# Kernel tuning notes

Hardware: AMD Instinct MI355X
Metric: run time of the kernel (lower is better)

The kernel has to match this reference:

```python
import jax, jax.numpy as jnp
import numpy as np

D_MODEL = 1024
N_HEADS = 16
D_HEAD = 64
TOTAL = N_HEADS * D_HEAD


def setup_inputs() -> dict:
    key = jax.random.key(0)
    k1, k2, k3 = jax.random.split(key, 3)
    x = jax.random.normal(k1, (2, 2048, D_MODEL), dtype=jnp.float32)
    W_qkv = jax.random.normal(k2, (3 * TOTAL, D_MODEL), dtype=jnp.float32) * 0.02
    W_out = jax.random.normal(k3, (D_MODEL, TOTAL), dtype=jnp.float32) * 0.02
    return {"x": x, "W_qkv": W_qkv, "W_out": W_out}


def reference(x, W_qkv, W_out):
    B, T, D = x.shape
    scale = D_HEAD ** -0.5
    qkv = jnp.einsum('btd,ed->bte', x, W_qkv)  # [B,T,3*TOTAL]
    q, k, v = jnp.split(qkv, 3, axis=-1)
    def heads(t):
        return t.reshape(B, T, N_HEADS, D_HEAD).transpose(0, 2, 1, 3)  # [B,H,T,Dh]
    q, k, v = heads(q), heads(k), heads(v)
    scores = jnp.einsum('bhqd,bhkd->bhqk', q, k) * scale
    causal = jnp.tril(jnp.ones((T, T), dtype=bool))
    scores = jnp.where(causal[None, None], scores, -jnp.inf)
    attn = jax.nn.softmax(scores, axis=-1)
    out = jnp.einsum('bhqk,bhkd->bhqd', attn, v)
    out = out.transpose(0, 2, 1, 3).reshape(B, T, TOTAL)
    return jnp.einsum('bte,de->btd', out, W_out)
```

## Files before the change

### kernel.cpp

```cpp
#include <hip/hip_runtime.h>
#include <hip/hip_bf16.h>

typedef __attribute__((ext_vector_type(4))) float f32x4;
typedef __attribute__((ext_vector_type(8))) short s16x8;
typedef __attribute__((ext_vector_type(4))) short s16x4;

#define DEV static __device__ __forceinline__

DEV unsigned short f2bf(float f) {
    unsigned int u = __builtin_bit_cast(unsigned int, f);
    u += 0x7fffu + ((u >> 16) & 1u);
    return (unsigned short)(u >> 16);
}

#if __has_builtin(__builtin_amdgcn_exp2f)
#define EXP2(x) __builtin_amdgcn_exp2f(x)
#else
#define EXP2(x) exp2f(x)
#endif

DEV unsigned int pack2(float a, float b) {
#if __has_builtin(__builtin_amdgcn_perm)
    return __builtin_amdgcn_perm(__builtin_bit_cast(unsigned int, b),
                                 __builtin_bit_cast(unsigned int, a), 0x07060302u);
#else
    return (__builtin_bit_cast(unsigned int, a) >> 16) |
           (__builtin_bit_cast(unsigned int, b) & 0xffff0000u);
#endif
}

DEV s16x8 ld8(const unsigned short* p) {
    s16x4 lo = *(const s16x4*)(p);
    s16x4 hi = *(const s16x4*)(p + 4);
    return __builtin_shufflevector(lo, hi, 0, 1, 2, 3, 4, 5, 6, 7);
}
DEV s16x8 ld8a(const unsigned short* p) { return *(const s16x8*)p; }

DEV f32x4 mfma16(s16x8 a, s16x8 b, f32x4 c) {
    return __builtin_amdgcn_mfma_f32_16x16x32_bf16(a, b, c, 0, 0, 0);
}

DEV void glds16(const unsigned short* g, unsigned short* l) {
    __builtin_amdgcn_global_load_lds(
        (const __attribute__((address_space(1))) unsigned int*)g,
        (__attribute__((address_space(3))) unsigned int*)l, 16, 0, 0);
}

__global__ __launch_bounds__(256) void convf2b3(
        const float* __restrict__ s0, unsigned short* __restrict__ d0, int n40,
        const float* __restrict__ s1, unsigned short* __restrict__ d1, int n41,
        const float* __restrict__ s2, unsigned short* __restrict__ d2, int n42) {
    int i = blockIdx.x * 256 + threadIdx.x;
    if (i < n40) {
        float4 v = ((const float4*)s0)[i];
        s16x4 o = {(short)f2bf(v.x), (short)f2bf(v.y), (short)f2bf(v.z), (short)f2bf(v.w)};
        ((s16x4*)d0)[i] = o;
    } else if (i - n40 < n41) {
        int j = i - n40;
        float4 v = ((const float4*)s1)[j];
        s16x4 o = {(short)f2bf(v.x), (short)f2bf(v.y), (short)f2bf(v.z), (short)f2bf(v.w)};
        ((s16x4*)d1)[j] = o;
    } else if (i - n40 - n41 < n42) {
        int j = i - n40 - n41;
        float4 v = ((const float4*)s2)[j];
        s16x4 o = {(short)f2bf(v.x), (short)f2bf(v.y), (short)f2bf(v.z), (short)f2bf(v.w)};
        ((s16x4*)d2)[j] = o;
    }
}

__global__ __launch_bounds__(256) void convf2b(const float* __restrict__ s,
                                               unsigned short* __restrict__ d, int n4) {
    int i = blockIdx.x * 256 + threadIdx.x;
    if (i < n4) {
        float4 v = ((const float4*)s)[i];
        s16x4 o = {(short)f2bf(v.x), (short)f2bf(v.y), (short)f2bf(v.z), (short)f2bf(v.w)};
        ((s16x4*)d)[i] = o;
    }
}

__global__ __launch_bounds__(512) void qkv_gemm(
        const unsigned short* __restrict__ Xb, const unsigned short* __restrict__ Wq,
        unsigned short* __restrict__ q_ws, unsigned short* __restrict__ k_ws,
        unsigned short* __restrict__ v_ws) {
    __shared__ unsigned short As[2][128 * 32];
    __shared__ unsigned short Bs[2][128 * 32];
    const int tid = threadIdx.x, lane = tid & 63, wave = tid >> 6;
    const int l15 = lane & 15, l4 = lane >> 4;
    const int wm = (wave >> 1) * 32, wn = (wave & 1) * 64;
    const int m0 = blockIdx.y * 128, n0 = blockIdx.x * 128;

    f32x4 acc[2][4];
    for (int i = 0; i < 2; i++)
        for (int j = 0; j < 4; j++) acc[i][j] = (f32x4){0.f, 0.f, 0.f, 0.f};

    const unsigned short* aptr = &Xb[(size_t)(m0 + wave * 16 + (lane >> 2)) * 1024 + (lane & 3) * 8];
    const unsigned short* bptr = &Wq[(size_t)(n0 + wave * 16 + (lane >> 2)) * 1024 + (lane & 3) * 8];

    for (int k0 = 0; k0 < 1024; k0 += 64) {
        __syncthreads();
        for (int c = 0; c < 2; c++) {
            glds16(aptr + k0 + c * 32, &As[c][(wave * 16) * 32]);
            glds16(bptr + k0 + c * 32, &Bs[c][(wave * 16) * 32]);
        }
        __syncthreads();
        for (int c = 0; c < 2; c++) {
            s16x8 af[2], bf[4];
            for (int mt = 0; mt < 2; mt++) af[mt] = ld8a(&As[c][(wm + mt * 16 + l15) * 32 + l4 * 8]);
            for (int nt = 0; nt < 4; nt++) bf[nt] = ld8a(&Bs[c][(wn + nt * 16 + l15) * 32 + l4 * 8]);
            for (int mt = 0; mt < 2; mt++)
                for (int nt = 0; nt < 4; nt++)
                    acc[mt][nt] = mfma16(af[mt], bf[nt], acc[mt][nt]);
        }
    }

    const int gnb = n0 + wn;
    const int which = gnb >> 10, h = (gnb >> 6) & 15;
    const int bidx = m0 >> 11, tb = m0 & 2047;
    if (which == 2) {
        unsigned short* dst = v_ws + (size_t)(bidx * 16 + h) * 64 * 2048;
        for (int mt = 0; mt < 2; mt++) {
            int t = tb + wm + mt * 16 + l4 * 4;
            for (int nt = 0; nt < 4; nt++) {
                int dh = nt * 16 + l15;
                s16x4 pp;
                for (int r = 0; r < 4; r++) pp[r] = (short)f2bf(acc[mt][nt][r]);
                *(s16x4*)&dst[(size_t)dh * 2048 + t] = pp;
            }
        }
    } else {
        unsigned short* dst = ((which == 0) ? q_ws : k_ws) + (size_t)(bidx * 16 + h) * 2048 * 64;
        const float sc = (which == 0) ? 0.18033688f : 1.0f;
        for (int mt = 0; mt < 2; mt++) {
            int t0 = tb + wm + mt * 16 + l4 * 4;
            for (int nt = 0; nt < 4; nt++) {
                int dh = nt * 16 + l15;
                for (int r = 0; r < 4; r++)
                    dst[(size_t)(t0 + r) * 64 + dh] = f2bf(acc[mt][nt][r] * sc);
            }
        }
    }
}

__global__ __launch_bounds__(512, 2) void attn(
        const unsigned short* __restrict__ q_ws, const unsigned short* __restrict__ k_ws,
        const unsigned short* __restrict__ v_ws, unsigned short* __restrict__ ao) {
    constexpr int LDP = 68;
    __shared__ unsigned short lds[66560];
    unsigned short* KsA = lds;
    unsigned short* VtA = lds + 12288;
    unsigned short* KsB = lds + 24576;
    unsigned short* VtB = lds + 36864;
    unsigned short* Ps  = lds + 49152;

    const int tid = threadIdx.x, lane = tid & 63, wave = tid >> 6;
    const int l15 = lane & 15, l4 = lane >> 4;
    const int xf = (l15 >> 1) & 3;

    const int id = blockIdx.x;
    const int bh8 = id & 7, rest = id >> 3;
    const int p = rest & 7, g = rest >> 3;
    const int bh = bh8 + 8 * g, b = bh >> 4, h = bh & 15;
    const bool isA = wave < 4;
    const int w4 = wave & 3;
    const int qrow_hi = (15 - p) * 128 + w4 * 32;
    const int qrow_lo = p * 128 + w4 * 32;
    const int Tlo = 2 * p + 2;

    const size_t base = (size_t)bh * 2048 * 64;
    const unsigned short* vtb = v_ws + (size_t)bh * 64 * 2048;
    unsigned short* Pw = &Ps[wave * 32 * LDP];

    const int seg = w4, srow = lane >> 2;
    const int scol = ((lane & 3) ^ ((lane >> 3) & 3)) * 8;
    const unsigned short* kg = &k_ws[base + (size_t)(seg * 16 + srow) * 64 + scol];
    const unsigned short* vg = &vtb[(size_t)(seg * 16 + srow) * 2048 + scol];
    unsigned short* Ksm = isA ? KsA : KsB;
    unsigned short* Vtm = isA ? VtA : VtB;

    auto stage = [&](int tau, int buf) {
        const unsigned short* kgt = kg + (size_t)tau * 4096;
        const unsigned short* vgt = vg + tau * 64;
        unsigned short* kd = Ksm + buf * 4096 + seg * 512;
        unsigned short* vd = Vtm + buf * 4096 + seg * 512;
        glds16(kgt,      kd);
        glds16(kgt + 32, kd + 2048);
        glds16(vgt,      vd);
        glds16(vgt + 32, vd + 2048);
    };
    auto myTile = [&](int x) { return (isA || x < Tlo) ? x : 17 + x - Tlo; };

    s16x8 qfh[2][2], qfl[2][2];
#pragma unroll
    for (int qs = 0; qs < 2; qs++)
#pragma unroll
        for (int c = 0; c < 2; c++)
            qfh[qs][c] = ld8a(&q_ws[base + (size_t)(qrow_hi + qs * 16 + l15) * 64 + c * 32 + l4 * 8]);
    if (!isA) {
#pragma unroll
        for (int qs = 0; qs < 2; qs++)
#pragma unroll
            for (int c = 0; c < 2; c++)
                qfl[qs][c] = ld8a(&q_ws[base + (size_t)(qrow_lo + qs * 16 + l15) * 64 + c * 32 + l4 * 8]);
    }
    asm volatile("s_waitcnt vmcnt(0)" ::: "memory");

    f32x4 oh[2][4], ol[2][4];
    float lh[2] = {0.f, 0.f}, ll[2] = {0.f, 0.f};
#pragma unroll
    for (int qs = 0; qs < 2; qs++)
#pragma unroll
        for (int i = 0; i < 4; i++) {
            oh[qs][i] = (f32x4){0.f, 0.f, 0.f, 0.f};
            ol[qs][i] = (f32x4){0.f, 0.f, 0.f, 0.f};
        }

    auto compute = [&](const unsigned short* kb, const unsigned short* vb,
                       s16x8 (&qf)[2][2], f32x4 (&o)[2][4], float (&ls)[2],
                       int qrow, int k0) {
        f32x4 st[2][4];
#pragma unroll
        for (int qs = 0; qs < 2; qs++)
#pragma unroll
            for (int ks = 0; ks < 4; ks++) st[qs][ks] = (f32x4){0.f, 0.f, 0.f, 0.f};
        __builtin_amdgcn_s_setprio(1);
#pragma unroll
        for (int c = 0; c < 2; c++)
#pragma unroll
            for (int ks = 0; ks < 4; ks++) {
                s16x8 kf = ld8a(&kb[c * 2048 + (ks * 16 + l15) * 32 + (l4 ^ xf) * 8]);
                st[0][ks] = mfma16(kf, qf[0][c], st[0][ks]);
                st[1][ks] = mfma16(kf, qf[1][c], st[1][ks]);
            }
        __builtin_amdgcn_s_setprio(0);

#pragma unroll
        for (int qs = 0; qs < 2; qs++) {
            const int qb = qrow + qs * 16;
            if (k0 + 63 > qb) {
                int qg = qb + l15;
#pragma unroll
                for (int ks = 0; ks < 4; ks++)
#pragma unroll
                    for (int rr = 0; rr < 4; rr++) {
                        int kgi = k0 + ks * 16 + l4 * 4 + rr;
                        if (kgi > qg) st[qs][ks][rr] = -1e30f;
                    }
            }
            float part = 0.f;
#pragma unroll
            for (int ks = 0; ks < 4; ks++) {
                float p0 = EXP2(st[qs][ks][0]);
                float p1 = EXP2(st[qs][ks][1]);
                float p2 = EXP2(st[qs][ks][2]);
                float p3 = EXP2(st[qs][ks][3]);
                part += (p0 + p1) + (p2 + p3);
                unsigned int u0 = pack2(p0, p1), u1 = pack2(p2, p3);
                *(uint2*)&Pw[(qs * 16 + l15) * LDP + ks * 16 + l4 * 4] = (uint2){u0, u1};
            }
            ls[qs] += part;
        }

        s16x8 pf[2][2];
#pragma unroll
        for (int qs = 0; qs < 2; qs++)
#pragma unroll
            for (int c = 0; c < 2; c++)
                pf[qs][c] = ld8(&Pw[(qs * 16 + l15) * LDP + c * 32 + l4 * 8]);
        __builtin_amdgcn_s_setprio(1);
#pragma unroll
        for (int c = 0; c < 2; c++)
#pragma unroll
            for (int ds = 0; ds < 4; ds++) {
                s16x8 vf = ld8a(&vb[c * 2048 + (ds * 16 + l15) * 32 + (l4 ^ xf) * 8]);
                o[0][ds] = mfma16(vf, pf[0][c], o[0][ds]);
                o[1][ds] = mfma16(vf, pf[1][c], o[1][ds]);
            }
        __builtin_amdgcn_s_setprio(0);
    };

    stage(myTile(0), 0);
    stage(myTile(1), 1);

    for (int r = 0; r < 17; ++r) {
        if (r < 16) asm volatile("s_waitcnt vmcnt(4)" ::: "memory");
        else        asm volatile("s_waitcnt vmcnt(0)" ::: "memory");
        __builtin_amdgcn_s_barrier();
        if (r + 2 < 17) stage(myTile(r + 2), (r + 2) % 3);
        const unsigned short* kb = Ksm + (r % 3) * 4096;
        const unsigned short* vb = Vtm + (r % 3) * 4096;
        if (isA) {
            compute(kb, vb, qfh, oh, lh, qrow_hi, r * 64);
        } else if (r < Tlo) {
            if (r * 64 < qrow_lo + 16) compute(kb, vb, qfl, ol, ll, qrow_lo, r * 64);
        } else {
            const int k0 = (17 + r - Tlo) * 64;
            if (k0 < qrow_hi + 16) compute(kb, vb, qfh, oh, lh, qrow_hi, k0);
        }
    }

    __syncthreads();
    float* mrg = (float*)lds;
    f32x4* m4 = (f32x4*)mrg;
    if (!isA) {
#pragma unroll
        for (int qs = 0; qs < 2; qs++) {
#pragma unroll
            for (int ds = 0; ds < 4; ds++)
                m4[w4 * 544 + (qs * 4 + ds) * 64 + lane] = oh[qs][ds];
            mrg[w4 * 2176 + 2048 + qs * 64 + lane] = lh[qs];
        }
    }
    __syncthreads();

    auto epilogue = [&](f32x4 (&o)[2][4], float (&ls)[2], int qrow) {
#pragma unroll
        for (int qs = 0; qs < 2; qs++) {
            float t = ls[qs];
            t += __shfl_xor(t, 16, 64);
            t += __shfl_xor(t, 32, 64);
            float inv = 1.f / t;
#pragma unroll
            for (int ds = 0; ds < 4; ds++) {
                s16x4 pp;
#pragma unroll
                for (int r = 0; r < 4; r++) pp[r] = (short)f2bf(o[qs][ds][r] * inv);
                *(s16x4*)&Pw[(qs * 16 + l15) * LDP + ds * 16 + l4 * 4] = pp;
            }
        }
        int qr = lane >> 2, qt = lane & 3;
#pragma unroll
        for (int qs = 0; qs < 2; qs++) {
            size_t orow = ((size_t)b * 2048 + qrow + qs * 16 + qr) * 1024 + h * 64 + qt * 16;
            *(s16x8*)&ao[orow]     = ld8(&Pw[(qs * 16 + qr) * LDP + qt * 16]);
            *(s16x8*)&ao[orow + 8] = ld8(&Pw[(qs * 16 + qr) * LDP + qt * 16 + 8]);
        }
    };

    if (isA) {
#pragma unroll
        for (int qs = 0; qs < 2; qs++) {
#pragma unroll
            for (int ds = 0; ds < 4; ds++)
                oh[qs][ds] += m4[w4 * 544 + (qs * 4 + ds) * 64 + lane];
            lh[qs] += mrg[w4 * 2176 + 2048 + qs * 64 + lane];
        }
        epilogue(oh, lh, qrow_hi);
    } else {
        epilogue(ol, ll, qrow_lo);
    }
}

__global__ __launch_bounds__(256) void out_gemm(
        const unsigned short* __restrict__ A, const unsigned short* __restrict__ Bm,
        float* __restrict__ OUT) {
    __shared__ unsigned short As[2][64 * 32];
    __shared__ unsigned short Bs[2][128 * 32];
    const int tid = threadIdx.x, lane = tid & 63, wave = tid >> 6;
    const int l15 = lane & 15, l4 = lane >> 4;
    const int wm = (wave >> 1) * 32, wn = (wave & 1) * 64;
    const int m0 = blockIdx.y * 64, n0 = blockIdx.x * 128;

    f32x4 acc[2][4];
    for (int i = 0; i < 2; i++)
        for (int j = 0; j < 4; j++) acc[i][j] = (f32x4){0.f, 0.f, 0.f, 0.f};

    const unsigned short* aptr = &A[(size_t)(m0 + wave * 16 + (lane >> 2)) * 1024 + (lane & 3) * 8];
    const unsigned short* bptr = &Bm[(size_t)(n0 + wave * 32 + (lane >> 2)) * 1024 + (lane & 3) * 8];

    for (int k0 = 0; k0 < 1024; k0 += 64) {
        __syncthreads();
        for (int c = 0; c < 2; c++) {
            glds16(aptr + k0 + c * 32, &As[c][(wave * 16) * 32]);
            glds16(bptr + k0 + c * 32, &Bs[c][(wave * 32) * 32]);
            glds16(bptr + k0 + c * 32 + 16 * 1024, &Bs[c][(wave * 32 + 16) * 32]);
        }
        __syncthreads();
        for (int c = 0; c < 2; c++) {
            s16x8 af[2], bf[4];
            for (int mt = 0; mt < 2; mt++) af[mt] = ld8a(&As[c][(wm + mt * 16 + l15) * 32 + l4 * 8]);
            for (int nt = 0; nt < 4; nt++) bf[nt] = ld8a(&Bs[c][(wn + nt * 16 + l15) * 32 + l4 * 8]);
            for (int mt = 0; mt < 2; mt++)
                for (int nt = 0; nt < 4; nt++)
                    acc[mt][nt] = mfma16(af[mt], bf[nt], acc[mt][nt]);
        }
    }

    for (int mt = 0; mt < 2; mt++)
        for (int nt = 0; nt < 4; nt++)
            for (int r = 0; r < 4; r++) {
                int gm = m0 + wm + mt * 16 + l4 * 4 + r;
                int gn = n0 + wn + nt * 16 + l15;
                OUT[(size_t)gm * 1024 + gn] = acc[mt][nt][r];
            }
}

extern "C" void kernel_launch(void* const* d_in, const int* in_sizes, int n_in,
                              void* d_out, int out_size, void* d_ws, size_t ws_size,
                              hipStream_t stream) {
    (void)in_sizes; (void)n_in; (void)out_size;
    const float* x    = (const float*)d_in[0];
    const float* Wqkv = (const float*)d_in[1];
    const float* Wout = (const float*)d_in[2];
    float* out = (float*)d_out;

    unsigned short* q_ws = (unsigned short*)d_ws;
    unsigned short* k_ws = q_ws + (size_t)4 * 1024 * 1024;
    unsigned short* v_ws = k_ws + (size_t)4 * 1024 * 1024;
    unsigned short* xb   = v_ws + (size_t)4 * 1024 * 1024;
    unsigned short* ao   = xb;
    unsigned short* wqb  = (unsigned short*)d_out;

    const int n4x = 2 * 2048 * 1024 / 4, n4w = 3072 * 1024 / 4, n4o = 1024 * 1024 / 4;
    const bool merged = ws_size >= (size_t)35 * 1024 * 1024;
    unsigned short* wob = merged ? (q_ws + (size_t)16 * 1024 * 1024)
                                 : q_ws;

    if (merged) {
        convf2b3<<<(n4x + n4w + n4o + 255) / 256, 256, 0, stream>>>(
            x, xb, n4x, Wqkv, wqb, n4w, Wout, wob, n4o);
    } else {
        convf2b3<<<(n4x + n4w + 255) / 256, 256, 0, stream>>>(
            x, xb, n4x, Wqkv, wqb, n4w, Wout, wob, 0);
    }
    qkv_gemm<<<dim3(24, 32), 512, 0, stream>>>(xb, wqb, q_ws, k_ws, v_ws);
    attn<<<dim3(256), 512, 0, stream>>>(q_ws, k_ws, v_ws, ao);
    if (!merged) convf2b<<<1024, 256, 0, stream>>>(Wout, wob, n4o);
    out_gemm<<<dim3(8, 64), 256, 0, stream>>>(ao, wob, out);
}
```

Measured before the change: 162.3 us.

## Stage K/V in double-buffered pairs of 64-key tiles and swizzle P scratch

The attention loop now loads two 64-key K/V tiles per stage into two double-buffered halves. This cuts the number of barrier/waitcnt rounds from 17 to 9, with a full vmcnt(0) drain each round. The per-wave P scratch drops from padded 32x68 rows to a single 16x64 XOR-swizzled tile that is reused per q-subtile, which reduces LDS bank conflicts. LDS grows to 144KB, and the full drain each round may expose more load latency than the previous 3-buffer rolling prefetch.

```diff
diff --git a/kernel.cpp b/kernel.cpp
--- a/kernel.cpp
+++ b/kernel.cpp
@@ -144,17 +144,17 @@
 __global__ __launch_bounds__(512, 2) void attn(
         const unsigned short* __restrict__ q_ws, const unsigned short* __restrict__ k_ws,
         const unsigned short* __restrict__ v_ws, unsigned short* __restrict__ ao) {
-    constexpr int LDP = 68;
-    __shared__ unsigned short lds[66560];
+    __shared__ unsigned short lds[73728];
     unsigned short* KsA = lds;
-    unsigned short* VtA = lds + 12288;
-    unsigned short* KsB = lds + 24576;
-    unsigned short* VtB = lds + 36864;
-    unsigned short* Ps  = lds + 49152;
+    unsigned short* VtA = lds + 16384;
+    unsigned short* KsB = lds + 32768;
+    unsigned short* VtB = lds + 49152;
+    unsigned short* Ps  = lds + 65536;
 
     const int tid = threadIdx.x, lane = tid & 63, wave = tid >> 6;
     const int l15 = lane & 15, l4 = lane >> 4;
     const int xf = (l15 >> 1) & 3;
+    const int sw = (l15 & 7) << 3;
 
     const int id = blockIdx.x;
     const int bh8 = id & 7, rest = id >> 3;
@@ -168,7 +168,7 @@
 
     const size_t base = (size_t)bh * 2048 * 64;
     const unsigned short* vtb = v_ws + (size_t)bh * 64 * 2048;
-    unsigned short* Pw = &Ps[wave * 32 * LDP];
+    unsigned short* Pw = &Ps[wave * 1024];
 
     const int seg = w4, srow = lane >> 2;
     const int scol = ((lane & 3) ^ ((lane >> 3) & 3)) * 8;
@@ -177,17 +177,17 @@
     unsigned short* Ksm = isA ? KsA : KsB;
     unsigned short* Vtm = isA ? VtA : VtB;
 
-    auto stage = [&](int tau, int buf) {
-        const unsigned short* kgt = kg + (size_t)tau * 4096;
-        const unsigned short* vgt = vg + tau * 64;
-        unsigned short* kd = Ksm + buf * 4096 + seg * 512;
-        unsigned short* vd = Vtm + buf * 4096 + seg * 512;
+    auto myTile = [&](int x) { return (isA || x < Tlo) ? x : 17 + x - Tlo; };
+    auto stage64 = [&](int t64, int buf, int sub) {
+        const unsigned short* kgt = kg + (size_t)t64 * 4096;
+        const unsigned short* vgt = vg + t64 * 64;
+        unsigned short* kd = Ksm + buf * 8192 + sub * 4096 + seg * 512;
+        unsigned short* vd = Vtm + buf * 8192 + sub * 4096 + seg * 512;
         glds16(kgt,      kd);
         glds16(kgt + 32, kd + 2048);
         glds16(vgt,      vd);
         glds16(vgt + 32, vd + 2048);
     };
-    auto myTile = [&](int x) { return (isA || x < Tlo) ? x : 17 + x - Tlo; };
 
     s16x8 qfh[2][2], qfl[2][2];
 #pragma unroll
@@ -233,6 +233,7 @@
             }
         __builtin_amdgcn_s_setprio(0);
 
+        s16x8 pf[2][2];
 #pragma unroll
         for (int qs = 0; qs < 2; qs++) {
             const int qb = qrow + qs * 16;
@@ -255,17 +256,14 @@
                 float p3 = EXP2(st[qs][ks][3]);
                 part += (p0 + p1) + (p2 + p3);
                 unsigned int u0 = pack2(p0, p1), u1 = pack2(p2, p3);
-                *(uint2*)&Pw[(qs * 16 + l15) * LDP + ks * 16 + l4 * 4] = (uint2){u0, u1};
+                *(uint2*)&Pw[l15 * 64 + ((ks * 16 + l4 * 4) ^ sw)] = (uint2){u0, u1};
             }
             ls[qs] += part;
-        }
-
-        s16x8 pf[2][2];
-#pragma unroll
-        for (int qs = 0; qs < 2; qs++)
 #pragma unroll
             for (int c = 0; c < 2; c++)
-                pf[qs][c] = ld8(&Pw[(qs * 16 + l15) * LDP + c * 32 + l4 * 8]);
+                pf[qs][c] = ld8(&Pw[l15 * 64 + ((c * 32 + l4 * 8) ^ sw)]);
+        }
+
         __builtin_amdgcn_s_setprio(1);
 #pragma unroll
         for (int c = 0; c < 2; c++)
@@ -278,23 +276,34 @@
         __builtin_amdgcn_s_setprio(0);
     };
 
-    stage(myTile(0), 0);
-    stage(myTile(1), 1);
-
-    for (int r = 0; r < 17; ++r) {
-        if (r < 16) asm volatile("s_waitcnt vmcnt(4)" ::: "memory");
+    stage64(myTile(0), 0, 0);
+    stage64(myTile(1), 0, 1);
+    stage64(myTile(2), 1, 0);
+    stage64(myTile(3), 1, 1);
+
+    for (int r = 0; r < 9; ++r) {
+        if (r == 0) asm volatile("s_waitcnt vmcnt(8)" ::: "memory");
         else        asm volatile("s_waitcnt vmcnt(0)" ::: "memory");
         __builtin_amdgcn_s_barrier();
-        if (r + 2 < 17) stage(myTile(r + 2), (r + 2) % 3);
-        const unsigned short* kb = Ksm + (r % 3) * 4096;
-        const unsigned short* vb = Vtm + (r % 3) * 4096;
-        if (isA) {
-            compute(kb, vb, qfh, oh, lh, qrow_hi, r * 64);
-        } else if (r < Tlo) {
-            if (r * 64 < qrow_lo + 16) compute(kb, vb, qfl, ol, ll, qrow_lo, r * 64);
-        } else {
-            const int k0 = (17 + r - Tlo) * 64;
-            if (k0 < qrow_hi + 16) compute(kb, vb, qfh, oh, lh, qrow_hi, k0);
+        if (r >= 1 && r + 1 <= 8) {
+            const int nb = (r + 1) & 1;
+            stage64(myTile(2 * (r + 1)), nb, 0);
+            if (r + 1 < 8) stage64(myTile(2 * (r + 1) + 1), nb, 1);
+        }
+#pragma unroll
+        for (int j = 0; j < 2; ++j) {
+            const int i = 2 * r + j;
+            if (i > 16) break;
+            const unsigned short* kb = Ksm + (r & 1) * 8192 + j * 4096;
+            const unsigned short* vb = Vtm + (r & 1) * 8192 + j * 4096;
+            const int k0 = myTile(i) * 64;
+            if (isA) {
+                if (k0 < qrow_hi + 16) compute(kb, vb, qfh, oh, lh, qrow_hi, k0);
+            } else if (i < Tlo) {
+                if (k0 < qrow_lo + 16) compute(kb, vb, qfl, ol, ll, qrow_lo, k0);
+            } else {
+                if (k0 < qrow_hi + 16) compute(kb, vb, qfh, oh, lh, qrow_hi, k0);
+            }
         }
     }
 
@@ -313,6 +322,8 @@
     __syncthreads();
 
     auto epilogue = [&](f32x4 (&o)[2][4], float (&ls)[2], int qrow) {
+        int qr = lane >> 2, qt = lane & 3;
+        const int swr = (qr & 7) << 3;
 #pragma unroll
         for (int qs = 0; qs < 2; qs++) {
             float t = ls[qs];
@@ -324,15 +335,11 @@
                 s16x4 pp;
 #pragma unroll
                 for (int r = 0; r < 4; r++) pp[r] = (short)f2bf(o[qs][ds][r] * inv);
-                *(s16x4*)&Pw[(qs * 16 + l15) * LDP + ds * 16 + l4 * 4] = pp;
-            }
-        }
-        int qr = lane >> 2, qt = lane & 3;
-#pragma unroll
-        for (int qs = 0; qs < 2; qs++) {
+                *(s16x4*)&Pw[l15 * 64 + ((ds * 16 + l4 * 4) ^ sw)] = pp;
+            }
             size_t orow = ((size_t)b * 2048 + qrow + qs * 16 + qr) * 1024 + h * 64 + qt * 16;
-            *(s16x8*)&ao[orow]     = ld8(&Pw[(qs * 16 + qr) * LDP + qt * 16]);
-            *(s16x8*)&ao[orow + 8] = ld8(&Pw[(qs * 16 + qr) * LDP + qt * 16 + 8]);
+            *(s16x8*)&ao[orow]     = ld8(&Pw[qr * 64 + ((qt * 16) ^ swr)]);
+            *(s16x8*)&ao[orow + 8] = ld8(&Pw[qr * 64 + ((qt * 16 + 8) ^ swr)]);
         }
     };
 
```

Result: no change. 161.6 us (-0.4%).
